# Kernel optimization log

Hardware: AMD Instinct MI355X
Metric: run time of the kernel (lower is better)

Reference implementation:

```python
import jax, jax.numpy as jnp
import numpy as np

N_NODES = 100000
IN_CH = 256
HIDDEN = 256
N_EDGES = 500000


def setup_inputs() -> dict:
    key = jax.random.key(0)
    k_emb, k_ei, k_w1, k_w2 = jax.random.split(key, 4)
    embeddings = jax.random.normal(k_emb, (N_NODES, IN_CH), dtype=jnp.float32)
    edge_index = jax.random.randint(k_ei, (2, N_EDGES), 0, N_NODES, dtype=jnp.int64)
    # Linear(in*2, hidden) and Linear(hidden, 1) weights (stored input-major for x @ W)
    s1 = 1.0 / np.sqrt(2 * IN_CH)
    s2 = 1.0 / np.sqrt(HIDDEN)
    W1 = jax.random.uniform(k_w1, (2 * IN_CH, HIDDEN), dtype=jnp.float32, minval=-s1, maxval=s1)
    b1 = jnp.zeros((HIDDEN,), dtype=jnp.float32)
    W2 = jax.random.uniform(k_w2, (HIDDEN, 1), dtype=jnp.float32, minval=-s2, maxval=s2)
    b2 = jnp.zeros((1,), dtype=jnp.float32)
    return {"embeddings": embeddings, "edge_index": edge_index,
            "W1": W1, "b1": b1, "W2": W2, "b2": b2}


def reference(embeddings, edge_index, W1, b1, W2, b2):
    src, dst = edge_index[0], edge_index[1]
    # gather [E, in] twice, concat -> [E, 2*in]
    feats = jnp.concatenate([embeddings[src], embeddings[dst]], axis=-1)
    h = jax.nn.relu(feats @ W1 + b1)          # [E, hidden]
    scores = h @ W2 + b2                      # [E, 1]
    return scores.reshape(-1)
```

## Files before the change

### kernel.cpp

```cpp
#include <hip/hip_runtime.h>
#include <hip/hip_bf16.h>

#define NN   100000
#define EE   500000
#define MPAD 100096

using bf16x8 = __attribute__((ext_vector_type(8))) short;
using f32x4  = __attribute__((ext_vector_type(4))) float;
using u16x8  = __attribute__((ext_vector_type(8))) unsigned short;

__device__ __forceinline__ unsigned short f2bf(float f) {
  unsigned int x = __builtin_bit_cast(unsigned int, f);
  x += 0x7fffu + ((x >> 16) & 1u);
  return (unsigned short)(x >> 16);
}
__device__ __forceinline__ float bf2f(unsigned short u) {
  unsigned int x = ((unsigned int)u) << 16;
  return __builtin_bit_cast(float, x);
}
__device__ __forceinline__ unsigned short f2bh(float f) {
  return __builtin_bit_cast(unsigned short, __float2bfloat16(f));
}
__device__ __forceinline__ void glds16(const void* g, const void* l) {
  __builtin_amdgcn_global_load_lds((const __attribute__((address_space(1))) void*)g,
                                   (__attribute__((address_space(3))) void*)l, 16, 0, 0);
}

__global__ void wprep_kernel(const float* __restrict__ W1, unsigned short* __restrict__ WT) {
  int id = blockIdx.x * blockDim.x + threadIdx.x;
  if (id >= 512 * 32) return;
  int j  = id >> 5;
  int cg = id & 31;
  int jc = j & 255;
  int kb = (cg << 3) + ((j >= 256) ? 256 : 0);
  u16x8 v;
#pragma unroll
  for (int t = 0; t < 8; ++t)
    v[t] = f2bf(W1[(size_t)(kb + t) * 256 + jc]);
  *reinterpret_cast<u16x8*>(WT + (size_t)j * 256 + (cg << 3)) = v;
}

__global__ __launch_bounds__(256, 3) void gemm_pq(const float* __restrict__ emb,
                                                  const unsigned short* __restrict__ WT,
                                                  const float* __restrict__ b1,
                                                  unsigned short* __restrict__ R) {
  __shared__ unsigned short ldsA[2][128 * 32];
  __shared__ unsigned short ldsB[2][128 * 32];

  const int t    = threadIdx.x;
  const int lane = t & 63;
  const int wave = t >> 6;
  const int wrow = wave >> 1, wcol = wave & 1;
  const int bid = (int)blockIdx.x;
  const int lid = (bid & 7) * 391 + (bid >> 3);
  const int m0 = (lid >> 2) * 128;
  const int n0 = (lid & 3) * 128;

  const int a_r = t >> 1, a_h = t & 1;
  int arow_g = m0 + a_r; if (arow_g >= NN) arow_g = NN - 1;
  const float* aSrc = emb + (size_t)arow_g * 256 + (a_h << 4);
  const int a_s  = (a_r >> 1) & 3;
  const int aW0  = a_r * 32 + ((((a_h << 1) | 0) ^ a_s) << 3);
  const int aW1  = a_r * 32 + ((((a_h << 1) | 1) ^ a_s) << 3);

  size_t bOff[2]; int bLds[2];
#pragma unroll
  for (int i = 0; i < 2; ++i) {
    const int r  = wave * 32 + i * 16 + (lane >> 2);
    const int qp = lane & 3;
    const int g  = qp ^ ((r >> 1) & 3);
    bOff[i] = (size_t)(n0 + r) * 256 + (g << 3);
    bLds[i] = (wave * 32 + i * 16) * 32;
  }

  const int fr = lane & 15, fq = lane >> 4;
  int aoff[4], boff[4];
#pragma unroll
  for (int m = 0; m < 4; ++m) {
    const int r = wrow * 64 + 16 * m + fr;
    aoff[m] = r * 32 + ((fq ^ ((r >> 1) & 3)) << 3);
  }
#pragma unroll
  for (int n = 0; n < 4; ++n) {
    const int r = wcol * 64 + 16 * n + fr;
    boff[n] = r * 32 + ((fq ^ ((r >> 1) & 3)) << 3);
  }

  f32x4 acc[4][4] = {};
  float4 pA[4];

#define ALOAD(kb)                                                              \
  do {                                                                         \
    pA[0] = *(const float4*)(aSrc + (kb));                                     \
    pA[1] = *(const float4*)(aSrc + (kb) + 4);                                 \
    pA[2] = *(const float4*)(aSrc + (kb) + 8);                                 \
    pA[3] = *(const float4*)(aSrc + (kb) + 12);                                \
  } while (0)

#define AWRITE(buf)                                                            \
  do {                                                                         \
    u16x8 w0, w1;                                                              \
    w0[0] = f2bh(pA[0].x); w0[1] = f2bh(pA[0].y);                              \
    w0[2] = f2bh(pA[0].z); w0[3] = f2bh(pA[0].w);                              \
    w0[4] = f2bh(pA[1].x); w0[5] = f2bh(pA[1].y);                              \
    w0[6] = f2bh(pA[1].z); w0[7] = f2bh(pA[1].w);                              \
    w1[0] = f2bh(pA[2].x); w1[1] = f2bh(pA[2].y);                              \
    w1[2] = f2bh(pA[2].z); w1[3] = f2bh(pA[2].w);                              \
    w1[4] = f2bh(pA[3].x); w1[5] = f2bh(pA[3].y);                              \
    w1[6] = f2bh(pA[3].z); w1[7] = f2bh(pA[3].w);                              \
    *(u16x8*)&ldsA[(buf)][aW0] = w0;                                           \
    *(u16x8*)&ldsA[(buf)][aW1] = w1;                                           \
  } while (0)

#define BGLDS(buf, kb)                                                         \
  do {                                                                         \
    glds16(WT + bOff[0] + (kb), &ldsB[(buf)][bLds[0]]);                        \
    glds16(WT + bOff[1] + (kb), &ldsB[(buf)][bLds[1]]);                        \
  } while (0)

  ALOAD(0);
  AWRITE(0);
  BGLDS(0, 0);
  ALOAD(32);
  __syncthreads();

#pragma unroll
  for (int ks = 0; ks < 8; ++ks) {
    const int p = ks & 1;
    if (ks < 7) {
      BGLDS(p ^ 1, (ks + 1) * 32);
      AWRITE(p ^ 1);
      if (ks < 6) ALOAD((ks + 2) * 32);
    }
    bf16x8 av[4], bv[4];
#pragma unroll
    for (int m = 0; m < 4; ++m) av[m] = *(const bf16x8*)&ldsA[p][aoff[m]];
#pragma unroll
    for (int n = 0; n < 4; ++n) bv[n] = *(const bf16x8*)&ldsB[p][boff[n]];
#pragma unroll
    for (int m = 0; m < 4; ++m)
#pragma unroll
      for (int n = 0; n < 4; ++n)
        acc[m][n] = __builtin_amdgcn_mfma_f32_16x16x32_bf16(av[m], bv[n], acc[m][n], 0, 0, 0);
    if (ks < 7) __syncthreads();
  }

  float bn[4];
#pragma unroll
  for (int n = 0; n < 4; ++n) {
    const int c = n0 + wcol * 64 + 16 * n + fr;
    bn[n] = (c < 256) ? b1[c] : 0.f;
  }
#pragma unroll
  for (int m = 0; m < 4; ++m) {
    const int r0 = m0 + wrow * 64 + 16 * m + (fq << 2);
#pragma unroll
    for (int n = 0; n < 4; ++n) {
      const int c = n0 + wcol * 64 + 16 * n + fr;
#pragma unroll
      for (int i = 0; i < 4; ++i)
        R[(size_t)(r0 + i) * 512 + c] = f2bf(acc[m][n][i] + bn[n]);
    }
  }
#undef ALOAD
#undef AWRITE
#undef BGLDS
}

__global__ __launch_bounds__(256) void edge_kernel(const int* __restrict__ idx,
                                                   const unsigned short* __restrict__ R,
                                                   const float* __restrict__ W2,
                                                   const float* __restrict__ b2,
                                                   float* __restrict__ out) {
  const int lane  = threadIdx.x & 63;
  const int half  = lane >> 5;
  const int l     = lane & 31;
  const int gwave = (int)((blockIdx.x * blockDim.x + threadIdx.x) >> 6);
  const int nwave = (int)((gridDim.x * blockDim.x) >> 6);
  const float4 w0 = *(const float4*)(W2 + (l << 3));
  const float4 w1 = *(const float4*)(W2 + (l << 3) + 4);
  const float bias = b2[0];

  for (int c = gwave; c < (EE / 8); c += nwave) {
    const int e0 = c << 3;
    int s[4], d[4];
#pragma unroll
    for (int u = 0; u < 4; ++u) {
      s[u] = idx[e0 + (u << 1) + half];
      d[u] = idx[EE + e0 + (u << 1) + half];
    }
    u16x8 ga[4], gb[4];
#pragma unroll
    for (int u = 0; u < 4; ++u) {
      ga[u] = *(const u16x8*)(R + (size_t)s[u] * 512 + (l << 3));
      gb[u] = *(const u16x8*)(R + (size_t)d[u] * 512 + 256 + (l << 3));
    }
#pragma unroll
    for (int u = 0; u < 4; ++u) {
      float acc;
      acc  = fmaxf(bf2f((unsigned short)ga[u][0]) + bf2f((unsigned short)gb[u][0]), 0.f) * w0.x;
      acc += fmaxf(bf2f((unsigned short)ga[u][1]) + bf2f((unsigned short)gb[u][1]), 0.f) * w0.y;
      acc += fmaxf(bf2f((unsigned short)ga[u][2]) + bf2f((unsigned short)gb[u][2]), 0.f) * w0.z;
      acc += fmaxf(bf2f((unsigned short)ga[u][3]) + bf2f((unsigned short)gb[u][3]), 0.f) * w0.w;
      acc += fmaxf(bf2f((unsigned short)ga[u][4]) + bf2f((unsigned short)gb[u][4]), 0.f) * w1.x;
      acc += fmaxf(bf2f((unsigned short)ga[u][5]) + bf2f((unsigned short)gb[u][5]), 0.f) * w1.y;
      acc += fmaxf(bf2f((unsigned short)ga[u][6]) + bf2f((unsigned short)gb[u][6]), 0.f) * w1.z;
      acc += fmaxf(bf2f((unsigned short)ga[u][7]) + bf2f((unsigned short)gb[u][7]), 0.f) * w1.w;
#pragma unroll
      for (int off = 16; off > 0; off >>= 1) acc += __shfl_xor(acc, off, 64);
      if (l == 0) out[e0 + (u << 1) + half] = acc + bias;
    }
  }
}

__global__ __launch_bounds__(256) void fallback_kernel(const float* __restrict__ emb,
                                                       const int* __restrict__ idx,
                                                       const float* __restrict__ W1,
                                                       const float* __restrict__ b1,
                                                       const float* __restrict__ W2,
                                                       const float* __restrict__ b2,
                                                       float* __restrict__ out) {
  __shared__ float feats[512];
  __shared__ float red[256];
  const int t = threadIdx.x;
  for (int e = blockIdx.x; e < EE; e += gridDim.x) {
    __syncthreads();
    const int s = idx[e], d = idx[EE + e];
    feats[t]       = emb[(size_t)s * 256 + t];
    feats[256 + t] = emb[(size_t)d * 256 + t];
    __syncthreads();
    float h = b1[t];
    for (int k = 0; k < 512; ++k) h += feats[k] * W1[k * 256 + t];
    red[t] = fmaxf(h, 0.f) * W2[t];
    __syncthreads();
    for (int off = 128; off > 0; off >>= 1) {
      if (t < off) red[t] += red[t + off];
      __syncthreads();
    }
    if (t == 0) out[e] = red[0] + b2[0];
  }
}

extern "C" void kernel_launch(void* const* d_in, const int* in_sizes, int n_in,
                              void* d_out, int out_size, void* d_ws, size_t ws_size,
                              hipStream_t stream) {
  const float* emb = (const float*)d_in[0];
  const int*   idx = (const int*)d_in[1];
  const float* W1  = (const float*)d_in[2];
  const float* b1  = (const float*)d_in[3];
  const float* W2  = (const float*)d_in[4];
  const float* b2  = (const float*)d_in[5];
  float* out = (float*)d_out;

  const size_t wt_elems = (size_t)512 * 256;
  const size_t r_elems  = (size_t)MPAD * 512;
  const size_t need = (wt_elems + r_elems) * sizeof(unsigned short);

  if (ws_size < need) {
    fallback_kernel<<<4096, 256, 0, stream>>>(emb, idx, W1, b1, W2, b2, out);
    return;
  }

  unsigned short* WT = (unsigned short*)d_ws;
  unsigned short* R  = WT + wt_elems;

  wprep_kernel<<<64, 256, 0, stream>>>(W1, WT);
  gemm_pq<<<(MPAD / 128) * 4, 256, 0, stream>>>(emb, WT, b1, R);
  edge_kernel<<<2048, 256, 0, stream>>>(idx, R, W2, b2, out);
}
```

Baseline: 137.2 us.

## Stage full A tile in LDS upfront and stream B fragments from global into registers

The GEMM kernel used to double-buffer both A and B through LDS with a barrier every k-step. Now it loads and converts the whole 128x256 A tile into LDS once, then runs the k-loop with a single barrier. B fragments go straight from global memory into registers with a four-stage ring, and A fragments are register double-buffered. The aim is to drop the per-step barriers and the LDS traffic for B. In exchange it uses 64KB of LDS and more registers, and occupancy is lowered to 2 blocks per unit. All A loads are exposed up front.

```diff
diff --git a/kernel.cpp b/kernel.cpp
--- a/kernel.cpp
+++ b/kernel.cpp
@@ -20,10 +20,6 @@
 }
 __device__ __forceinline__ unsigned short f2bh(float f) {
   return __builtin_bit_cast(unsigned short, __float2bfloat16(f));
-}
-__device__ __forceinline__ void glds16(const void* g, const void* l) {
-  __builtin_amdgcn_global_load_lds((const __attribute__((address_space(1))) void*)g,
-                                   (__attribute__((address_space(3))) void*)l, 16, 0, 0);
 }
 
 __global__ void wprep_kernel(const float* __restrict__ W1, unsigned short* __restrict__ WT) {
@@ -40,12 +36,11 @@
   *reinterpret_cast<u16x8*>(WT + (size_t)j * 256 + (cg << 3)) = v;
 }
 
-__global__ __launch_bounds__(256, 3) void gemm_pq(const float* __restrict__ emb,
+__global__ __launch_bounds__(256, 2) void gemm_pq(const float* __restrict__ emb,
                                                   const unsigned short* __restrict__ WT,
                                                   const float* __restrict__ b1,
                                                   unsigned short* __restrict__ R) {
-  __shared__ unsigned short ldsA[2][128 * 32];
-  __shared__ unsigned short ldsB[2][128 * 32];
+  __shared__ unsigned short ldsA[8][128 * 32];
 
   const int t    = threadIdx.x;
   const int lane = t & 63;
@@ -59,90 +54,69 @@
   const int a_r = t >> 1, a_h = t & 1;
   int arow_g = m0 + a_r; if (arow_g >= NN) arow_g = NN - 1;
   const float* aSrc = emb + (size_t)arow_g * 256 + (a_h << 4);
-  const int a_s  = (a_r >> 1) & 3;
-  const int aW0  = a_r * 32 + ((((a_h << 1) | 0) ^ a_s) << 3);
-  const int aW1  = a_r * 32 + ((((a_h << 1) | 1) ^ a_s) << 3);
-
-  size_t bOff[2]; int bLds[2];
-#pragma unroll
-  for (int i = 0; i < 2; ++i) {
-    const int r  = wave * 32 + i * 16 + (lane >> 2);
-    const int qp = lane & 3;
-    const int g  = qp ^ ((r >> 1) & 3);
-    bOff[i] = (size_t)(n0 + r) * 256 + (g << 3);
-    bLds[i] = (wave * 32 + i * 16) * 32;
+  const int swzA = (a_r >> 1) & 3;
+  const int aW0  = a_r * 32 + ((((a_h << 1) | 0) ^ swzA) << 3);
+  const int aW1  = a_r * 32 + ((((a_h << 1) | 1) ^ swzA) << 3);
+#pragma unroll
+  for (int s = 0; s < 8; ++s) {
+    float4 f0 = *(const float4*)(aSrc + s * 32);
+    float4 f1 = *(const float4*)(aSrc + s * 32 + 4);
+    float4 f2 = *(const float4*)(aSrc + s * 32 + 8);
+    float4 f3 = *(const float4*)(aSrc + s * 32 + 12);
+    u16x8 w0, w1;
+    w0[0] = f2bh(f0.x); w0[1] = f2bh(f0.y); w0[2] = f2bh(f0.z); w0[3] = f2bh(f0.w);
+    w0[4] = f2bh(f1.x); w0[5] = f2bh(f1.y); w0[6] = f2bh(f1.z); w0[7] = f2bh(f1.w);
+    w1[0] = f2bh(f2.x); w1[1] = f2bh(f2.y); w1[2] = f2bh(f2.z); w1[3] = f2bh(f2.w);
+    w1[4] = f2bh(f3.x); w1[5] = f2bh(f3.y); w1[6] = f2bh(f3.z); w1[7] = f2bh(f3.w);
+    *(u16x8*)&ldsA[s][aW0] = w0;
+    *(u16x8*)&ldsA[s][aW1] = w1;
   }
 
   const int fr = lane & 15, fq = lane >> 4;
-  int aoff[4], boff[4];
+  int aoff[4];
 #pragma unroll
   for (int m = 0; m < 4; ++m) {
     const int r = wrow * 64 + 16 * m + fr;
     aoff[m] = r * 32 + ((fq ^ ((r >> 1) & 3)) << 3);
   }
-#pragma unroll
-  for (int n = 0; n < 4; ++n) {
-    const int r = wcol * 64 + 16 * n + fr;
-    boff[n] = r * 32 + ((fq ^ ((r >> 1) & 3)) << 3);
-  }
+  const unsigned short* bRow[4];
+#pragma unroll
+  for (int n = 0; n < 4; ++n)
+    bRow[n] = WT + (size_t)(n0 + wcol * 64 + 16 * n + fr) * 256 + (fq << 3);
+
+  bf16x8 bv[4][4];
+#pragma unroll
+  for (int s = 0; s < 4; ++s)
+#pragma unroll
+    for (int n = 0; n < 4; ++n)
+      bv[s][n] = *(const bf16x8*)(bRow[n] + (s << 5));
+
+  __syncthreads();
 
   f32x4 acc[4][4] = {};
-  float4 pA[4];
-
-#define ALOAD(kb)                                                              \
-  do {                                                                         \
-    pA[0] = *(const float4*)(aSrc + (kb));                                     \
-    pA[1] = *(const float4*)(aSrc + (kb) + 4);                                 \
-    pA[2] = *(const float4*)(aSrc + (kb) + 8);                                 \
-    pA[3] = *(const float4*)(aSrc + (kb) + 12);                                \
-  } while (0)
-
-#define AWRITE(buf)                                                            \
-  do {                                                                         \
-    u16x8 w0, w1;                                                              \
-    w0[0] = f2bh(pA[0].x); w0[1] = f2bh(pA[0].y);                              \
-    w0[2] = f2bh(pA[0].z); w0[3] = f2bh(pA[0].w);                              \
-    w0[4] = f2bh(pA[1].x); w0[5] = f2bh(pA[1].y);                              \
-    w0[6] = f2bh(pA[1].z); w0[7] = f2bh(pA[1].w);                              \
-    w1[0] = f2bh(pA[2].x); w1[1] = f2bh(pA[2].y);                              \
-    w1[2] = f2bh(pA[2].z); w1[3] = f2bh(pA[2].w);                              \
-    w1[4] = f2bh(pA[3].x); w1[5] = f2bh(pA[3].y);                              \
-    w1[6] = f2bh(pA[3].z); w1[7] = f2bh(pA[3].w);                              \
-    *(u16x8*)&ldsA[(buf)][aW0] = w0;                                           \
-    *(u16x8*)&ldsA[(buf)][aW1] = w1;                                           \
-  } while (0)
-
-#define BGLDS(buf, kb)                                                         \
-  do {                                                                         \
-    glds16(WT + bOff[0] + (kb), &ldsB[(buf)][bLds[0]]);                        \
-    glds16(WT + bOff[1] + (kb), &ldsB[(buf)][bLds[1]]);                        \
-  } while (0)
-
-  ALOAD(0);
-  AWRITE(0);
-  BGLDS(0, 0);
-  ALOAD(32);
-  __syncthreads();
+  bf16x8 av[2][4];
+#pragma unroll
+  for (int m = 0; m < 4; ++m) av[0][m] = *(const bf16x8*)&ldsA[0][aoff[m]];
 
 #pragma unroll
   for (int ks = 0; ks < 8; ++ks) {
-    const int p = ks & 1;
+    const int cur = ks & 1;
     if (ks < 7) {
-      BGLDS(p ^ 1, (ks + 1) * 32);
-      AWRITE(p ^ 1);
-      if (ks < 6) ALOAD((ks + 2) * 32);
-    }
-    bf16x8 av[4], bv[4];
-#pragma unroll
-    for (int m = 0; m < 4; ++m) av[m] = *(const bf16x8*)&ldsA[p][aoff[m]];
-#pragma unroll
-    for (int n = 0; n < 4; ++n) bv[n] = *(const bf16x8*)&ldsB[p][boff[n]];
+#pragma unroll
+      for (int m = 0; m < 4; ++m)
+        av[cur ^ 1][m] = *(const bf16x8*)&ldsA[ks + 1][aoff[m]];
+    }
 #pragma unroll
     for (int m = 0; m < 4; ++m)
 #pragma unroll
       for (int n = 0; n < 4; ++n)
-        acc[m][n] = __builtin_amdgcn_mfma_f32_16x16x32_bf16(av[m], bv[n], acc[m][n], 0, 0, 0);
-    if (ks < 7) __syncthreads();
+        acc[m][n] = __builtin_amdgcn_mfma_f32_16x16x32_bf16(av[cur][m], bv[ks & 3][n],
+                                                            acc[m][n], 0, 0, 0);
+    if (ks < 4) {
+#pragma unroll
+      for (int n = 0; n < 4; ++n)
+        bv[ks & 3][n] = *(const bf16x8*)(bRow[n] + ((ks + 4) << 5));
+    }
   }
 
   float bn[4];
@@ -159,12 +133,9 @@
       const int c = n0 + wcol * 64 + 16 * n + fr;
 #pragma unroll
       for (int i = 0; i < 4; ++i)
-        R[(size_t)(r0 + i) * 512 + c] = f2bf(acc[m][n][i] + bn[n]);
-    }
-  }
-#undef ALOAD
-#undef AWRITE
-#undef BGLDS
+        R[(size_t)(r0 + i) * 512 + c] = f2bh(acc[m][n][i] + bn[n]);
+    }
+  }
 }
 
 __global__ __launch_bounds__(256) void edge_kernel(const int* __restrict__ idx,
```

Measured after the change: 162.5 us. 18.4% more time.

## Stage fp32 A tile via global_load_lds and convert to bf16 at fragment read

Applied to the files above, without the earlier changes.

The GEMM now loads the fp32 embedding tile directly into LDS with asynchronous global-to-LDS copies, the same path B already uses, instead of going through registers with a bf16 conversion before the LDS write. The conversion to bf16 moves to the point where MFMA fragments are read from LDS. This is meant to drop the register-staged A prefetch and its VGPR pressure and to overlap A loads with compute. In exchange LDS use for A doubles, which may reduce occupancy, LDS read traffic doubles, conversion runs redundantly per fragment read, and an extra barrier is added after the last iteration.

```diff
diff --git a/kernel.cpp b/kernel.cpp
--- a/kernel.cpp
+++ b/kernel.cpp
@@ -44,7 +44,7 @@
                                                   const unsigned short* __restrict__ WT,
                                                   const float* __restrict__ b1,
                                                   unsigned short* __restrict__ R) {
-  __shared__ unsigned short ldsA[2][128 * 32];
+  __shared__ float          ldsA[2][128 * 32];
   __shared__ unsigned short ldsB[2][128 * 32];
 
   const int t    = threadIdx.x;
@@ -56,13 +56,16 @@
   const int m0 = (lid >> 2) * 128;
   const int n0 = (lid & 3) * 128;
 
-  const int a_r = t >> 1, a_h = t & 1;
-  int arow_g = m0 + a_r; if (arow_g >= NN) arow_g = NN - 1;
-  const float* aSrc = emb + (size_t)arow_g * 256 + (a_h << 4);
-  const int a_s  = (a_r >> 1) & 3;
-  const int aW0  = a_r * 32 + ((((a_h << 1) | 0) ^ a_s) << 3);
-  const int aW1  = a_r * 32 + ((((a_h << 1) | 1) ^ a_s) << 3);
-
+  size_t aOff[4]; int aLds[4];
+#pragma unroll
+  for (int i = 0; i < 4; ++i) {
+    const int row = wave * 32 + i * 8 + (lane >> 3);
+    const int s   = (lane & 7) >> 1, h = lane & 1;
+    const int g   = s ^ ((row >> 1) & 3);
+    int rowg = m0 + row; if (rowg >= NN) rowg = NN - 1;
+    aOff[i] = (size_t)rowg * 256 + (g << 3) + (h << 2);
+    aLds[i] = wave * 1024 + i * 256;
+  }
   size_t bOff[2]; int bLds[2];
 #pragma unroll
   for (int i = 0; i < 2; ++i) {
@@ -86,55 +89,38 @@
     boff[n] = r * 32 + ((fq ^ ((r >> 1) & 3)) << 3);
   }
 
+#define STAGE(buf, ks)                                                         \
+  do {                                                                         \
+    glds16(emb + aOff[0] + ((ks) << 5), &ldsA[(buf)][aLds[0]]);                \
+    glds16(emb + aOff[1] + ((ks) << 5), &ldsA[(buf)][aLds[1]]);                \
+    glds16(emb + aOff[2] + ((ks) << 5), &ldsA[(buf)][aLds[2]]);                \
+    glds16(emb + aOff[3] + ((ks) << 5), &ldsA[(buf)][aLds[3]]);                \
+    glds16(WT + bOff[0] + ((ks) << 5), &ldsB[(buf)][bLds[0]]);                 \
+    glds16(WT + bOff[1] + ((ks) << 5), &ldsB[(buf)][bLds[1]]);                 \
+  } while (0)
+
   f32x4 acc[4][4] = {};
-  float4 pA[4];
-
-#define ALOAD(kb)                                                              \
-  do {                                                                         \
-    pA[0] = *(const float4*)(aSrc + (kb));                                     \
-    pA[1] = *(const float4*)(aSrc + (kb) + 4);                                 \
-    pA[2] = *(const float4*)(aSrc + (kb) + 8);                                 \
-    pA[3] = *(const float4*)(aSrc + (kb) + 12);                                \
-  } while (0)
-
-#define AWRITE(buf)                                                            \
-  do {                                                                         \
-    u16x8 w0, w1;                                                              \
-    w0[0] = f2bh(pA[0].x); w0[1] = f2bh(pA[0].y);                              \
-    w0[2] = f2bh(pA[0].z); w0[3] = f2bh(pA[0].w);                              \
-    w0[4] = f2bh(pA[1].x); w0[5] = f2bh(pA[1].y);                              \
-    w0[6] = f2bh(pA[1].z); w0[7] = f2bh(pA[1].w);                              \
-    w1[0] = f2bh(pA[2].x); w1[1] = f2bh(pA[2].y);                              \
-    w1[2] = f2bh(pA[2].z); w1[3] = f2bh(pA[2].w);                              \
-    w1[4] = f2bh(pA[3].x); w1[5] = f2bh(pA[3].y);                              \
-    w1[6] = f2bh(pA[3].z); w1[7] = f2bh(pA[3].w);                              \
-    *(u16x8*)&ldsA[(buf)][aW0] = w0;                                           \
-    *(u16x8*)&ldsA[(buf)][aW1] = w1;                                           \
-  } while (0)
-
-#define BGLDS(buf, kb)                                                         \
-  do {                                                                         \
-    glds16(WT + bOff[0] + (kb), &ldsB[(buf)][bLds[0]]);                        \
-    glds16(WT + bOff[1] + (kb), &ldsB[(buf)][bLds[1]]);                        \
-  } while (0)
-
-  ALOAD(0);
-  AWRITE(0);
-  BGLDS(0, 0);
-  ALOAD(32);
+
+  STAGE(0, 0);
   __syncthreads();
 
 #pragma unroll
   for (int ks = 0; ks < 8; ++ks) {
     const int p = ks & 1;
-    if (ks < 7) {
-      BGLDS(p ^ 1, (ks + 1) * 32);
-      AWRITE(p ^ 1);
-      if (ks < 6) ALOAD((ks + 2) * 32);
-    }
+    if (ks < 7) STAGE(p ^ 1, ks + 1);
     bf16x8 av[4], bv[4];
 #pragma unroll
-    for (int m = 0; m < 4; ++m) av[m] = *(const bf16x8*)&ldsA[p][aoff[m]];
+    for (int m = 0; m < 4; ++m) {
+      const float* pa = &ldsA[p][aoff[m]];
+      float4 x0 = *(const float4*)pa;
+      float4 x1 = *(const float4*)(pa + 4);
+      bf16x8 a;
+      a[0] = (short)f2bh(x0.x); a[1] = (short)f2bh(x0.y);
+      a[2] = (short)f2bh(x0.z); a[3] = (short)f2bh(x0.w);
+      a[4] = (short)f2bh(x1.x); a[5] = (short)f2bh(x1.y);
+      a[6] = (short)f2bh(x1.z); a[7] = (short)f2bh(x1.w);
+      av[m] = a;
+    }
 #pragma unroll
     for (int n = 0; n < 4; ++n) bv[n] = *(const bf16x8*)&ldsB[p][boff[n]];
 #pragma unroll
@@ -142,7 +128,7 @@
 #pragma unroll
       for (int n = 0; n < 4; ++n)
         acc[m][n] = __builtin_amdgcn_mfma_f32_16x16x32_bf16(av[m], bv[n], acc[m][n], 0, 0, 0);
-    if (ks < 7) __syncthreads();
+    __syncthreads();
   }
 
   float bn[4];
@@ -159,12 +145,10 @@
       const int c = n0 + wcol * 64 + 16 * n + fr;
 #pragma unroll
       for (int i = 0; i < 4; ++i)
-        R[(size_t)(r0 + i) * 512 + c] = f2bf(acc[m][n][i] + bn[n]);
-    }
-  }
-#undef ALOAD
-#undef AWRITE
-#undef BGLDS
+        R[(size_t)(r0 + i) * 512 + c] = f2bh(acc[m][n][i] + bn[n]);
+    }
+  }
+#undef STAGE
 }
 
 __global__ __launch_bounds__(256) void edge_kernel(const int* __restrict__ idx,
```

Result: slower. 164.0 us (+19.5%).

## Triple-buffer LDS and deepen A-prefetch pipeline in node GEMM

Applied to the files above, without the earlier changes.

The node-projection GEMM moves from double to triple-buffered LDS. It now keeps two register sets of A prefetched, so global fp32 loads for the slices two or three steps ahead are in flight during MFMA compute. Explicit s_waitcnt vmcnt counts, raw s_barrier and sched_barrier fences replace __syncthreads, so only the data needed for the current stage is waited on. This raises LDS use and register pressure, which could cut occupancy under launch_bounds(256,3), and the hand-tuned wait counts carry a correctness risk. The output conversion also switches from the manual round to the intrinsic bf16 conversion.

```diff
diff --git a/kernel.cpp b/kernel.cpp
--- a/kernel.cpp
+++ b/kernel.cpp
@@ -44,8 +44,8 @@
                                                   const unsigned short* __restrict__ WT,
                                                   const float* __restrict__ b1,
                                                   unsigned short* __restrict__ R) {
-  __shared__ unsigned short ldsA[2][128 * 32];
-  __shared__ unsigned short ldsB[2][128 * 32];
+  __shared__ unsigned short ldsA[3][128 * 32];
+  __shared__ unsigned short ldsB[3][128 * 32];
 
   const int t    = threadIdx.x;
   const int lane = t & 63;
@@ -87,63 +87,85 @@
   }
 
   f32x4 acc[4][4] = {};
-  float4 pA[4];
-
-#define ALOAD(kb)                                                              \
-  do {                                                                         \
-    pA[0] = *(const float4*)(aSrc + (kb));                                     \
-    pA[1] = *(const float4*)(aSrc + (kb) + 4);                                 \
-    pA[2] = *(const float4*)(aSrc + (kb) + 8);                                 \
-    pA[3] = *(const float4*)(aSrc + (kb) + 12);                                \
-  } while (0)
-
-#define AWRITE(buf)                                                            \
+  float4 pX[4], pY[4];
+
+#define ALOAD(reg, slice)                                                      \
+  do {                                                                         \
+    reg[0] = *(const float4*)(aSrc + ((slice) << 5));                          \
+    reg[1] = *(const float4*)(aSrc + ((slice) << 5) + 4);                      \
+    reg[2] = *(const float4*)(aSrc + ((slice) << 5) + 8);                      \
+    reg[3] = *(const float4*)(aSrc + ((slice) << 5) + 12);                     \
+  } while (0)
+
+#define AWRITE(buf, reg)                                                       \
   do {                                                                         \
     u16x8 w0, w1;                                                              \
-    w0[0] = f2bh(pA[0].x); w0[1] = f2bh(pA[0].y);                              \
-    w0[2] = f2bh(pA[0].z); w0[3] = f2bh(pA[0].w);                              \
-    w0[4] = f2bh(pA[1].x); w0[5] = f2bh(pA[1].y);                              \
-    w0[6] = f2bh(pA[1].z); w0[7] = f2bh(pA[1].w);                              \
-    w1[0] = f2bh(pA[2].x); w1[1] = f2bh(pA[2].y);                              \
-    w1[2] = f2bh(pA[2].z); w1[3] = f2bh(pA[2].w);                              \
-    w1[4] = f2bh(pA[3].x); w1[5] = f2bh(pA[3].y);                              \
-    w1[6] = f2bh(pA[3].z); w1[7] = f2bh(pA[3].w);                              \
+    w0[0] = f2bh(reg[0].x); w0[1] = f2bh(reg[0].y);                            \
+    w0[2] = f2bh(reg[0].z); w0[3] = f2bh(reg[0].w);                            \
+    w0[4] = f2bh(reg[1].x); w0[5] = f2bh(reg[1].y);                            \
+    w0[6] = f2bh(reg[1].z); w0[7] = f2bh(reg[1].w);                            \
+    w1[0] = f2bh(reg[2].x); w1[1] = f2bh(reg[2].y);                            \
+    w1[2] = f2bh(reg[2].z); w1[3] = f2bh(reg[2].w);                            \
+    w1[4] = f2bh(reg[3].x); w1[5] = f2bh(reg[3].y);                            \
+    w1[6] = f2bh(reg[3].z); w1[7] = f2bh(reg[3].w);                            \
     *(u16x8*)&ldsA[(buf)][aW0] = w0;                                           \
     *(u16x8*)&ldsA[(buf)][aW1] = w1;                                           \
   } while (0)
 
-#define BGLDS(buf, kb)                                                         \
-  do {                                                                         \
-    glds16(WT + bOff[0] + (kb), &ldsB[(buf)][bLds[0]]);                        \
-    glds16(WT + bOff[1] + (kb), &ldsB[(buf)][bLds[1]]);                        \
-  } while (0)
-
-  ALOAD(0);
-  AWRITE(0);
-  BGLDS(0, 0);
-  ALOAD(32);
-  __syncthreads();
-
-#pragma unroll
-  for (int ks = 0; ks < 8; ++ks) {
-    const int p = ks & 1;
-    if (ks < 7) {
-      BGLDS(p ^ 1, (ks + 1) * 32);
-      AWRITE(p ^ 1);
-      if (ks < 6) ALOAD((ks + 2) * 32);
-    }
-    bf16x8 av[4], bv[4];
-#pragma unroll
-    for (int m = 0; m < 4; ++m) av[m] = *(const bf16x8*)&ldsA[p][aoff[m]];
-#pragma unroll
-    for (int n = 0; n < 4; ++n) bv[n] = *(const bf16x8*)&ldsB[p][boff[n]];
-#pragma unroll
-    for (int m = 0; m < 4; ++m)
-#pragma unroll
-      for (int n = 0; n < 4; ++n)
-        acc[m][n] = __builtin_amdgcn_mfma_f32_16x16x32_bf16(av[m], bv[n], acc[m][n], 0, 0, 0);
-    if (ks < 7) __syncthreads();
-  }
+#define BGLDS(buf, slice)                                                      \
+  do {                                                                         \
+    glds16(WT + bOff[0] + ((slice) << 5), &ldsB[(buf)][bLds[0]]);              \
+    glds16(WT + bOff[1] + ((slice) << 5), &ldsB[(buf)][bLds[1]]);              \
+  } while (0)
+
+#define COMPUTE(p)                                                             \
+  do {                                                                         \
+    bf16x8 av[4], bv[4];                                                       \
+    _Pragma("unroll")                                                          \
+    for (int m = 0; m < 4; ++m) av[m] = *(const bf16x8*)&ldsA[(p)][aoff[m]];   \
+    _Pragma("unroll")                                                          \
+    for (int n = 0; n < 4; ++n) bv[n] = *(const bf16x8*)&ldsB[(p)][boff[n]];   \
+    _Pragma("unroll")                                                          \
+    for (int m = 0; m < 4; ++m)                                                \
+      _Pragma("unroll")                                                        \
+      for (int n = 0; n < 4; ++n)                                              \
+        acc[m][n] = __builtin_amdgcn_mfma_f32_16x16x32_bf16(av[m], bv[n],      \
+                                                            acc[m][n], 0, 0, 0); \
+  } while (0)
+
+#define SB() __builtin_amdgcn_sched_barrier(0)
+
+#define STEP(ks, preg, NW)                                                     \
+  do {                                                                         \
+    if ((ks) < 7) { AWRITE((ks + 1) % 3, preg); }                              \
+    SB();                                                                      \
+    if ((ks) < 7) { BGLDS((ks + 1) % 3, (ks) + 1); }                           \
+    SB();                                                                      \
+    if ((ks) <= 4) { ALOAD(preg, (ks) + 3); }                                  \
+    SB();                                                                      \
+    asm volatile("s_waitcnt vmcnt(" #NW ") lgkmcnt(0)" ::: "memory");          \
+    __builtin_amdgcn_s_barrier();                                              \
+    SB();                                                                      \
+    COMPUTE((ks) % 3);                                                         \
+  } while (0)
+
+  ALOAD(pX, 0); SB();
+  ALOAD(pY, 1); SB();
+  AWRITE(0, pX); SB();
+  BGLDS(0, 0); SB();
+  ALOAD(pX, 2); SB();
+  asm volatile("s_waitcnt vmcnt(4) lgkmcnt(0)" ::: "memory");
+  __builtin_amdgcn_s_barrier();
+  SB();
+
+  STEP(0, pY, 10);
+  STEP(1, pX, 10);
+  STEP(2, pY, 10);
+  STEP(3, pX, 10);
+  STEP(4, pY, 10);
+  STEP(5, pX, 6);
+  STEP(6, pY, 2);
+  STEP(7, pX, 0);
 
   float bn[4];
 #pragma unroll
@@ -159,12 +181,15 @@
       const int c = n0 + wcol * 64 + 16 * n + fr;
 #pragma unroll
       for (int i = 0; i < 4; ++i)
-        R[(size_t)(r0 + i) * 512 + c] = f2bf(acc[m][n][i] + bn[n]);
+        R[(size_t)(r0 + i) * 512 + c] = f2bh(acc[m][n][i] + bn[n]);
     }
   }
 #undef ALOAD
 #undef AWRITE
 #undef BGLDS
+#undef COMPUTE
+#undef STEP
+#undef SB
 }
 
 __global__ __launch_bounds__(256) void edge_kernel(const int* __restrict__ idx,
```

New measurement: 136.8 us. No clear change (-0.3%).
